# Kernel tuning notes

Hardware: AMD Instinct MI355X
Metric: run time of the kernel (lower is better)

Reference implementation:

```python
import jax, jax.numpy as jnp
import numpy as np

B, S, D, H = 4, 2048, 1024, 16
HD = D // H


def setup_inputs() -> dict:
    key = jax.random.key(0)
    k1, k2, k3 = jax.random.split(key, 3)
    x = jax.random.normal(k1, (B, S, D), dtype=jnp.float32)
    w_qkv = jax.random.normal(k2, (D, 3 * D), dtype=jnp.float32) * (1.0 / np.sqrt(D))
    w_out = jax.random.normal(k3, (D, D), dtype=jnp.float32) * (1.0 / np.sqrt(D))
    return {"x": x, "w_qkv": w_qkv, "w_out": w_out}


def reference(x, w_qkv, w_out):
    bsz, seq_len, d = x.shape
    qkv = x @ w_qkv  # [B, S, 3D]
    q, k, v = jnp.split(qkv, 3, axis=-1)
    # [B, H, S, HD]
    q = q.reshape(bsz, seq_len, H, HD).transpose(0, 2, 1, 3)
    k = k.reshape(bsz, seq_len, H, HD).transpose(0, 2, 1, 3)
    v = v.reshape(bsz, seq_len, H, HD).transpose(0, 2, 1, 3)
    scale = 1.0 / np.sqrt(HD)
    scores = jnp.einsum('bhqd,bhkd->bhqk', q, k) * scale  # [B, H, S, S]
    causal = jnp.tril(jnp.ones((seq_len, seq_len), dtype=bool))
    scores = jnp.where(causal[None, None], scores, -jnp.inf)
    weights = jax.nn.softmax(scores, axis=-1)
    ctx = jnp.einsum('bhqk,bhkd->bhqd', weights, v)
    ctx = ctx.transpose(0, 2, 1, 3).reshape(bsz, seq_len, d)
    return ctx @ w_out
```

## Files before the change

### kernel.cpp

```cpp
#include <hip/hip_runtime.h>
#include <stdint.h>

typedef unsigned short u16;
typedef __attribute__((ext_vector_type(4))) float f32x4;
typedef __attribute__((ext_vector_type(16))) float f32x16;
typedef __attribute__((ext_vector_type(8))) __bf16 bf16x8;
typedef __attribute__((ext_vector_type(8))) u16 u16x8;
typedef __attribute__((ext_vector_type(4))) u16 u16x4;

static constexpr int kB = 4, kS = 2048, kD = 1024, kH = 16, kHD = 64;
static constexpr int M1 = kB * kS;
static constexpr int N1 = 3 * kD;
static constexpr int K1 = kD;

#define SCLF 0.18033688011112042f
#define MFMA32(a, b, c) __builtin_amdgcn_mfma_f32_32x32x16_bf16((a), (b), (c), 0, 0, 0)

union U4 { unsigned u[4]; bf16x8 v; };

__device__ __forceinline__ u16 f2bf(float f) {
  union { float f; uint32_t u; } c; c.f = f;
  uint32_t u = c.u + 0x7FFFu + ((c.u >> 16) & 1u);
  return (u16)(u >> 16);
}

__device__ __forceinline__ unsigned pkbf(float a, float b) {
  union { __bf16 h[2]; unsigned u; } c;
  c.h[0] = (__bf16)a; c.h[1] = (__bf16)b;
  return c.u;
}

__device__ __forceinline__ f32x16 zero16() {
  f32x16 v;
#pragma unroll
  for (int i = 0; i < 16; ++i) v[i] = 0.f;
  return v;
}

__device__ __forceinline__ void gload_lds16(const u16* g, u16* l) {
  __builtin_amdgcn_global_load_lds(
      (const __attribute__((address_space(1))) unsigned int*)g,
      (__attribute__((address_space(3))) unsigned int*)l, 16, 0, 0);
}

__device__ __forceinline__ void packP(const float* pp, int hi, U4& f0, U4& f1) {
  const unsigned qa0 = pkbf(pp[0], pp[1]),   qa1 = pkbf(pp[2], pp[3]);
  const unsigned qb0 = pkbf(pp[4], pp[5]),   qb1 = pkbf(pp[6], pp[7]);
  const unsigned qc0 = pkbf(pp[8], pp[9]),   qc1 = pkbf(pp[10], pp[11]);
  const unsigned qd0 = pkbf(pp[12], pp[13]), qd1 = pkbf(pp[14], pp[15]);
  const unsigned xa0 = __shfl_xor(qa0, 32, 64), xa1 = __shfl_xor(qa1, 32, 64);
  const unsigned xb0 = __shfl_xor(qb0, 32, 64), xb1 = __shfl_xor(qb1, 32, 64);
  const unsigned xc0 = __shfl_xor(qc0, 32, 64), xc1 = __shfl_xor(qc1, 32, 64);
  const unsigned xd0 = __shfl_xor(qd0, 32, 64), xd1 = __shfl_xor(qd1, 32, 64);
  f0.u[0] = hi ? xb0 : qa0; f0.u[1] = hi ? xb1 : qa1;
  f0.u[2] = hi ? qb0 : xa0; f0.u[3] = hi ? qb1 : xa1;
  f1.u[0] = hi ? xd0 : qc0; f1.u[1] = hi ? xd1 : qc1;
  f1.u[2] = hi ? qd0 : xc0; f1.u[3] = hi ? qd1 : xc1;
}

__global__ __launch_bounds__(256) void k_cast_x(const float* __restrict__ x,
                                                u16* __restrict__ o) {
  int i = (blockIdx.x * 256 + threadIdx.x) * 4;
  f32x4 v = *(const f32x4*)(x + i);
  u16x4 r;
  r[0] = f2bf(v[0]); r[1] = f2bf(v[1]); r[2] = f2bf(v[2]); r[3] = f2bf(v[3]);
  *(u16x4*)(o + i) = r;
}

__global__ __launch_bounds__(256) void k_transpose_cast(const float* __restrict__ w,
                                                        u16* __restrict__ wt,
                                                        int K, int N) {
  __shared__ float t[32][33];
  const int n0 = blockIdx.x * 32, k0 = blockIdx.y * 32;
  const int tx = threadIdx.x & 31, ty = threadIdx.x >> 5;
  for (int r = ty; r < 32; r += 8)
    t[r][tx] = w[(size_t)(k0 + r) * N + n0 + tx];
  __syncthreads();
  for (int r = ty; r < 32; r += 8)
    wt[(size_t)(n0 + r) * K + k0 + tx] = f2bf(t[tx][r]);
}

template <int MODE>
__global__ __launch_bounds__(256) void k_gemm_bt(const u16* __restrict__ A,
                                                 const u16* __restrict__ BT,
                                                 u16* __restrict__ obf,
                                                 float* __restrict__ of,
                                                 int M, int N, int K) {
  typedef __attribute__((ext_vector_type(4))) float f4;
  __shared__ __align__(16) u16 As[128 * 32];
  __shared__ __align__(16) u16 Bs[128 * 32];
  const int tid = threadIdx.x;
  const int wave = tid >> 6, lane = tid & 63;
  const int l15 = lane & 15, l16 = lane >> 4;
  const int row0 = blockIdx.y * 128, col0 = blockIdx.x * 128;
  const int wm = (wave >> 1) * 64, wn = (wave & 1) * 64;

  f4 acc[4][4];
#pragma unroll
  for (int i = 0; i < 4; ++i)
#pragma unroll
    for (int j = 0; j < 4; ++j) acc[i][j] = f4{0.f, 0.f, 0.f, 0.f};

  const int e0 = wave * 512 + lane * 8;
  const int r0 = e0 >> 5, c0 = e0 & 31;
  const int e1 = e0 + 2048;
  const int r1 = e1 >> 5, c1 = e1 & 31;
  const u16* Ab = A + (size_t)row0 * K;
  const u16* Bb = BT + (size_t)col0 * K;

  for (int kt = 0; kt < K; kt += 32) {
    gload_lds16(Ab + (size_t)r0 * K + kt + c0, &As[wave * 512]);
    gload_lds16(Ab + (size_t)r1 * K + kt + c1, &As[2048 + wave * 512]);
    gload_lds16(Bb + (size_t)r0 * K + kt + c0, &Bs[wave * 512]);
    gload_lds16(Bb + (size_t)r1 * K + kt + c1, &Bs[2048 + wave * 512]);
    __syncthreads();
    bf16x8 af[4], bfv[4];
#pragma unroll
    for (int f = 0; f < 4; ++f) {
      af[f]  = *(const bf16x8*)&As[(wm + f * 16 + l15) * 32 + l16 * 8];
      bfv[f] = *(const bf16x8*)&Bs[(wn + f * 16 + l15) * 32 + l16 * 8];
    }
#pragma unroll
    for (int fm = 0; fm < 4; ++fm)
#pragma unroll
      for (int fn = 0; fn < 4; ++fn)
        acc[fm][fn] = __builtin_amdgcn_mfma_f32_16x16x32_bf16(af[fm], bfv[fn],
                                                              acc[fm][fn], 0, 0, 0);
    __syncthreads();
  }

#pragma unroll
  for (int fm = 0; fm < 4; ++fm)
#pragma unroll
    for (int fn = 0; fn < 4; ++fn) {
      const int n = col0 + wn + fn * 16 + l15;
#pragma unroll
      for (int j = 0; j < 4; ++j) {
        const int m = row0 + wm + fm * 16 + l16 * 4 + j;
        float v = acc[fm][fn][j];
        if constexpr (MODE == 0) {
          const int which = n >> 10, d = n & 1023;
          const int h = d >> 6, hd = d & 63;
          const int b = m >> 11, s = m & 2047;
          if (which == 0) v *= SCLF;
          obf[((((size_t)which * 4 + b) * 16 + h) * 2048 + s) * 64 + hd] = f2bf(v);
        } else {
          of[(size_t)m * N + n] = v;
        }
      }
    }
}

__global__ __launch_bounds__(256, 2) void k_attn(const u16* __restrict__ Qg,
                                                 const u16* __restrict__ Kg,
                                                 const u16* __restrict__ Vg,
                                                 u16* __restrict__ ctx) {
  __shared__ __align__(16) u16 Ks[2][128 * 64];
  __shared__ __align__(16) unsigned Vt[2][64 * 64];

  const int p = blockIdx.x, bh = blockIdx.y;
  const int bb = bh >> 4, hh = bh & 15;
  const int tid = threadIdx.x;
  const int wave = tid >> 6, lane = tid & 63;
  const int l31 = lane & 31, hi = lane >> 5;

  const u16* Qb = Qg + (size_t)bh * kS * kHD;
  const u16* Kb = Kg + (size_t)bh * kS * kHD;
  const u16* Vb = Vg + (size_t)bh * kS * kHD;

  const int do8 = tid & 7, kpw = tid >> 3;
  const int kkey8 = lane >> 3, ksl = lane & 7;
  const int swzA = (((l31 & 7) ^ (l31 >> 3)) << 2);

  for (int phase = 0; phase < 2; ++phase) {
    const int qsup = phase ? (15 - p) : p;
    const int s0 = qsup * 128;
    const int qstart = s0 + wave * 32;
    const int ntiles = qsup + 1;

    bf16x8 bq[4];
#pragma unroll
    for (int ds = 0; ds < 4; ++ds)
      bq[ds] = *(const bf16x8*)(Qb + (size_t)(qstart + l31) * 64 + ds * 16 + hi * 8);

    f32x16 acco0 = zero16(), acco1 = zero16();
    float mrow = -3e38f, lrowh = 0.f;

    __syncthreads();

    u16x8 va[2], vb[2];
#pragma unroll
    for (int r = 0; r < 2; ++r) {
      const u16* vs = Vb + (size_t)(2 * (kpw + 32 * r)) * 64 + do8 * 8;
      va[r] = *(const u16x8*)vs; vb[r] = *(const u16x8*)(vs + 64);
    }
#pragma unroll
    for (int r = 0; r < 2; ++r)
#pragma unroll
      for (int i = 0; i < 8; ++i) {
        const int d = do8 * 8 + i;
        Vt[0][d * 64 + ((kpw + 32 * r) ^ ((((d & 7) ^ (d >> 3))) << 2))] =
            (unsigned)va[r][i] | ((unsigned)vb[r][i] << 16);
      }
#pragma unroll
    for (int r = 0; r < 2; ++r) {
      const u16* vs = Vb + (size_t)(128 + 2 * (kpw + 32 * r)) * 64 + do8 * 8;
      va[r] = *(const u16x8*)vs; vb[r] = *(const u16x8*)(vs + 64);
    }
#pragma unroll
    for (int r = 0; r < 4; ++r) {
      const int key = wave * 32 + r * 8 + kkey8;
      gload_lds16(Kb + (size_t)key * 64 + (ksl ^ (key & 7)) * 8,
                  &Ks[0][(wave * 4 + r) * 512]);
    }

    for (int t = 0; t < ntiles; ++t) {
      const int kv0 = t * 128;
      __syncthreads();

      if (t + 1 < ntiles) {
        const int nb = (t + 1) & 1;
#pragma unroll
        for (int r = 0; r < 2; ++r)
#pragma unroll
          for (int i = 0; i < 8; ++i) {
            const int d = do8 * 8 + i;
            Vt[nb][d * 64 + ((kpw + 32 * r) ^ ((((d & 7) ^ (d >> 3))) << 2))] =
                (unsigned)va[r][i] | ((unsigned)vb[r][i] << 16);
          }
#pragma unroll
        for (int r = 0; r < 4; ++r) {
          const int key = wave * 32 + r * 8 + kkey8;
          gload_lds16(Kb + (size_t)(kv0 + 128 + key) * 64 + (ksl ^ (key & 7)) * 8,
                      &Ks[nb][(wave * 4 + r) * 512]);
        }
        if (t + 2 < ntiles) {
#pragma unroll
          for (int r = 0; r < 2; ++r) {
            const u16* vs = Vb + (size_t)(kv0 + 256 + 2 * (kpw + 32 * r)) * 64 + do8 * 8;
            va[r] = *(const u16x8*)vs; vb[r] = *(const u16x8*)(vs + 64);
          }
        }
      }

      const u16* Ksb = &Ks[t & 1][0];
      const unsigned* Vtb = &Vt[t & 1][0];
      const int qv = qstart + l31;

#pragma unroll
      for (int h = 0; h < 2; ++h) {
        const int kb = kv0 + 64 * h;
        if (kb > qstart + 31) continue;
        const int krow = 64 * h;
        const bool pres1 = (kb + 32 <= qstart + 31);

        f32x16 st0 = zero16(), st1 = zero16();
        __builtin_amdgcn_s_setprio(1);
#pragma unroll
        for (int ds = 0; ds < 4; ++ds) {
          const int sl = (((ds << 1) | hi) ^ (l31 & 7)) * 8;
          bf16x8 ak0 = *(const bf16x8*)&Ksb[(krow + l31) * 64 + sl];
          st0 = MFMA32(ak0, bq[ds], st0);
          if (pres1) {
            bf16x8 ak1 = *(const bf16x8*)&Ksb[(krow + 32 + l31) * 64 + sl];
            st1 = MFMA32(ak1, bq[ds], st1);
          }
        }
        __builtin_amdgcn_s_setprio(0);

        float tl = -3e38f;
        if (kb + 31 > qstart) {
          const int kb0 = kb + 4 * hi;
#pragma unroll
          for (int r = 0; r < 16; ++r) {
            const int key = kb0 + (r & 3) + 8 * (r >> 2);
            float v = st0[r];
            v = (key <= qv) ? v : -3e38f;
            st0[r] = v;
            tl = fmaxf(tl, v);
          }
        } else {
#pragma unroll
          for (int r = 0; r < 16; ++r) tl = fmaxf(tl, st0[r]);
        }
        if (pres1) {
          if (kb + 63 > qstart) {
            const int kb1 = kb + 32 + 4 * hi;
#pragma unroll
            for (int r = 0; r < 16; ++r) {
              const int key = kb1 + (r & 3) + 8 * (r >> 2);
              float v = st1[r];
              v = (key <= qv) ? v : -3e38f;
              st1[r] = v;
              tl = fmaxf(tl, v);
            }
          } else {
#pragma unroll
            for (int r = 0; r < 16; ++r) tl = fmaxf(tl, st1[r]);
          }
        }

        float mn;
        if (__all(tl <= mrow + 8.0f)) {
          mn = mrow;
        } else {
          const float tj = fmaxf(tl, __shfl_xor(tl, 32, 64));
          mn = fmaxf(mrow, tj);
          const float al = exp2f(mrow - mn);
          mrow = mn;
          lrowh *= al;
#pragma unroll
          for (int r = 0; r < 16; ++r) { acco0[r] *= al; acco1[r] *= al; }
        }

        {
          float pp[16];
#pragma unroll
          for (int r = 0; r < 16; ++r) pp[r] = exp2f(st0[r] - mn);
          const float t0 = (pp[0] + pp[1]) + (pp[2] + pp[3]);
          const float t1 = (pp[4] + pp[5]) + (pp[6] + pp[7]);
          const float t2 = (pp[8] + pp[9]) + (pp[10] + pp[11]);
          const float t3 = (pp[12] + pp[13]) + (pp[14] + pp[15]);
          lrowh += (t0 + t1) + (t2 + t3);
          U4 f0, f1;
          packP(pp, hi, f0, f1);
          const int c0 = 32 * h;
          __builtin_amdgcn_s_setprio(1);
          {
            const int dbase = l31 * 64, sz = swzA;
            const bf16x8 vfa = *(const bf16x8*)&Vtb[dbase + ((c0 + hi * 4) ^ sz)];
            acco0 = MFMA32(vfa, f0.v, acco0);
            const bf16x8 vfb = *(const bf16x8*)&Vtb[dbase + ((c0 + 8 + hi * 4) ^ sz)];
            acco0 = MFMA32(vfb, f1.v, acco0);
          }
          {
            const int dbase = (32 + l31) * 64, sz = swzA ^ 16;
            const bf16x8 vfa = *(const bf16x8*)&Vtb[dbase + ((c0 + hi * 4) ^ sz)];
            acco1 = MFMA32(vfa, f0.v, acco1);
            const bf16x8 vfb = *(const bf16x8*)&Vtb[dbase + ((c0 + 8 + hi * 4) ^ sz)];
            acco1 = MFMA32(vfb, f1.v, acco1);
          }
          __builtin_amdgcn_s_setprio(0);
        }
        if (pres1) {
          float pp[16];
#pragma unroll
          for (int r = 0; r < 16; ++r) pp[r] = exp2f(st1[r] - mn);
          const float t0 = (pp[0] + pp[1]) + (pp[2] + pp[3]);
          const float t1 = (pp[4] + pp[5]) + (pp[6] + pp[7]);
          const float t2 = (pp[8] + pp[9]) + (pp[10] + pp[11]);
          const float t3 = (pp[12] + pp[13]) + (pp[14] + pp[15]);
          lrowh += (t0 + t1) + (t2 + t3);
          U4 f0, f1;
          packP(pp, hi, f0, f1);
          const int c1 = 32 * h + 16;
          __builtin_amdgcn_s_setprio(1);
          {
            const int dbase = l31 * 64, sz = swzA;
            const bf16x8 vfa = *(const bf16x8*)&Vtb[dbase + ((c1 + hi * 4) ^ sz)];
            acco0 = MFMA32(vfa, f0.v, acco0);
            const bf16x8 vfb = *(const bf16x8*)&Vtb[dbase + ((c1 + 8 + hi * 4) ^ sz)];
            acco0 = MFMA32(vfb, f1.v, acco0);
          }
          {
            const int dbase = (32 + l31) * 64, sz = swzA ^ 16;
            const bf16x8 vfa = *(const bf16x8*)&Vtb[dbase + ((c1 + hi * 4) ^ sz)];
            acco1 = MFMA32(vfa, f0.v, acco1);
            const bf16x8 vfb = *(const bf16x8*)&Vtb[dbase + ((c1 + 8 + hi * 4) ^ sz)];
            acco1 = MFMA32(vfb, f1.v, acco1);
          }
          __builtin_amdgcn_s_setprio(0);
        }
      }
    }

    const float lrow = lrowh + __shfl_xor(lrowh, 32, 64);
    const float rl = 1.0f / lrow;
    u16* orow = ctx + ((size_t)bb * kS + (qstart + l31)) * kD + hh * 64;
#pragma unroll
    for (int rq = 0; rq < 4; ++rq) {
      u16x4 pk0, pk1;
#pragma unroll
      for (int c = 0; c < 4; ++c) {
        pk0[c] = f2bf(acco0[rq * 4 + c] * rl);
        pk1[c] = f2bf(acco1[rq * 4 + c] * rl);
      }
      *(u16x4*)&orow[rq * 8 + hi * 4] = pk0;
      *(u16x4*)&orow[32 + rq * 8 + hi * 4] = pk1;
    }
  }
}

extern "C" void kernel_launch(void* const* d_in, const int* in_sizes, int n_in,
                              void* d_out, int out_size, void* d_ws, size_t ws_size,
                              hipStream_t stream) {
  const float* x     = (const float*)d_in[0];
  const float* w_qkv = (const float*)d_in[1];
  const float* w_out = (const float*)d_in[2];
  float* out = (float*)d_out;

  u16* ws    = (u16*)d_ws;
  u16* x_bf  = ws;
  u16* wqkvT = x_bf + (size_t)M1 * K1;
  u16* woutT = wqkvT + (size_t)N1 * K1;
  u16* qkv   = woutT + (size_t)kD * kD;
  u16* ctx   = qkv + (size_t)3 * kB * kH * kS * kHD;

  k_cast_x<<<M1 * K1 / 1024, 256, 0, stream>>>(x, x_bf);
  k_transpose_cast<<<dim3(N1 / 32, K1 / 32), 256, 0, stream>>>(w_qkv, wqkvT, K1, N1);
  k_transpose_cast<<<dim3(kD / 32, kD / 32), 256, 0, stream>>>(w_out, woutT, kD, kD);

  k_gemm_bt<0><<<dim3(N1 / 128, M1 / 128), 256, 0, stream>>>(x_bf, wqkvT, qkv, nullptr,
                                                             M1, N1, K1);

  const u16* Qg = qkv;
  const u16* Kg = qkv + (size_t)kB * kH * kS * kHD;
  const u16* Vg = qkv + (size_t)2 * kB * kH * kS * kHD;
  k_attn<<<dim3(8, kB * kH), 256, 0, stream>>>(Qg, Kg, Vg, ctx);

  k_gemm_bt<1><<<dim3(kD / 128, M1 / 128), 256, 0, stream>>>(ctx, woutT, nullptr, out,
                                                             M1, kD, K1);
}
```

Measured before the change: 212.0 us.

## Split attention into one block per query tile with XCD-aware ordering and smaller KV tiles

```diff
diff --git a/kernel.cpp b/kernel.cpp
--- a/kernel.cpp
+++ b/kernel.cpp
@@ -92,7 +92,11 @@
   const int tid = threadIdx.x;
   const int wave = tid >> 6, lane = tid & 63;
   const int l15 = lane & 15, l16 = lane >> 4;
-  const int row0 = blockIdx.y * 128, col0 = blockIdx.x * 128;
+
+  const int bid = blockIdx.y * gridDim.x + blockIdx.x;
+  const int qch = (gridDim.x * gridDim.y) >> 3;
+  const int swz = (bid & 7) * qch + (bid >> 3);
+  const int row0 = (swz / gridDim.x) * 128, col0 = (swz % gridDim.x) * 128;
   const int wm = (wave >> 1) * 64, wn = (wave & 1) * 64;
 
   f4 acc[4][4];
@@ -151,243 +155,225 @@
     }
 }
 
-__global__ __launch_bounds__(256, 2) void k_attn(const u16* __restrict__ Qg,
+__global__ __launch_bounds__(256, 4) void k_attn(const u16* __restrict__ Qg,
                                                  const u16* __restrict__ Kg,
                                                  const u16* __restrict__ Vg,
                                                  u16* __restrict__ ctx) {
-  __shared__ __align__(16) u16 Ks[2][128 * 64];
-  __shared__ __align__(16) unsigned Vt[2][64 * 64];
-
-  const int p = blockIdx.x, bh = blockIdx.y;
+  __shared__ __align__(16) u16 Ks[2][64 * 64];
+  __shared__ __align__(16) unsigned Vt[2][64 * 32];
+
+  const int bid = blockIdx.x;
+  const int xcd = bid & 7, idx = bid >> 3;
+  const int bh = xcd * 8 + (idx >> 4);
+  const int qsup = 15 - (idx & 15);
   const int bb = bh >> 4, hh = bh & 15;
   const int tid = threadIdx.x;
   const int wave = tid >> 6, lane = tid & 63;
   const int l31 = lane & 31, hi = lane >> 5;
+  const int s0 = qsup * 128;
+  const int qstart = s0 + wave * 32;
+  const int ntiles = 2 * qsup + 2;
 
   const u16* Qb = Qg + (size_t)bh * kS * kHD;
   const u16* Kb = Kg + (size_t)bh * kS * kHD;
   const u16* Vb = Vg + (size_t)bh * kS * kHD;
 
-  const int do8 = tid & 7, kpw = tid >> 3;
+  const int do8 = tid & 7, kp = tid >> 3;
   const int kkey8 = lane >> 3, ksl = lane & 7;
   const int swzA = (((l31 & 7) ^ (l31 >> 3)) << 2);
 
-  for (int phase = 0; phase < 2; ++phase) {
-    const int qsup = phase ? (15 - p) : p;
-    const int s0 = qsup * 128;
-    const int qstart = s0 + wave * 32;
-    const int ntiles = qsup + 1;
-
-    bf16x8 bq[4];
-#pragma unroll
-    for (int ds = 0; ds < 4; ++ds)
-      bq[ds] = *(const bf16x8*)(Qb + (size_t)(qstart + l31) * 64 + ds * 16 + hi * 8);
-
-    f32x16 acco0 = zero16(), acco1 = zero16();
-    float mrow = -3e38f, lrowh = 0.f;
-
+  unsigned voff[8];
+#pragma unroll
+  for (int i = 0; i < 8; ++i) {
+    const int d = do8 * 8 + i;
+    voff[i] = d * 32 + (kp ^ ((((d & 7) ^ (d >> 3))) << 2));
+  }
+
+  bf16x8 bq[4];
+#pragma unroll
+  for (int ds = 0; ds < 4; ++ds)
+    bq[ds] = *(const bf16x8*)(Qb + (size_t)(qstart + l31) * 64 + ds * 16 + hi * 8);
+
+  f32x16 acco0 = zero16(), acco1 = zero16();
+  float mrow = -3e38f, lrowh = 0.f;
+
+  u16x8 va, vb;
+  {
+    const u16* vs = Vb + (size_t)(2 * kp) * 64 + do8 * 8;
+    va = *(const u16x8*)vs; vb = *(const u16x8*)(vs + 64);
+  }
+#pragma unroll
+  for (int i = 0; i < 8; ++i)
+    Vt[0][voff[i]] = (unsigned)va[i] | ((unsigned)vb[i] << 16);
+  {
+    const u16* vs = Vb + (size_t)(64 + 2 * kp) * 64 + do8 * 8;
+    va = *(const u16x8*)vs; vb = *(const u16x8*)(vs + 64);
+  }
+#pragma unroll
+  for (int rep = 0; rep < 2; ++rep) {
+    const int key = wave * 16 + rep * 8 + kkey8;
+    gload_lds16(Kb + (size_t)key * 64 + (ksl ^ (key & 7)) * 8,
+                &Ks[0][(wave * 2 + rep) * 512]);
+  }
+
+  for (int t = 0; t < ntiles; ++t) {
+    const int kv0 = t * 64;
     __syncthreads();
 
-    u16x8 va[2], vb[2];
-#pragma unroll
-    for (int r = 0; r < 2; ++r) {
-      const u16* vs = Vb + (size_t)(2 * (kpw + 32 * r)) * 64 + do8 * 8;
-      va[r] = *(const u16x8*)vs; vb[r] = *(const u16x8*)(vs + 64);
-    }
-#pragma unroll
-    for (int r = 0; r < 2; ++r)
-#pragma unroll
-      for (int i = 0; i < 8; ++i) {
-        const int d = do8 * 8 + i;
-        Vt[0][d * 64 + ((kpw + 32 * r) ^ ((((d & 7) ^ (d >> 3))) << 2))] =
-            (unsigned)va[r][i] | ((unsigned)vb[r][i] << 16);
-      }
-#pragma unroll
-    for (int r = 0; r < 2; ++r) {
-      const u16* vs = Vb + (size_t)(128 + 2 * (kpw + 32 * r)) * 64 + do8 * 8;
-      va[r] = *(const u16x8*)vs; vb[r] = *(const u16x8*)(vs + 64);
-    }
-#pragma unroll
-    for (int r = 0; r < 4; ++r) {
-      const int key = wave * 32 + r * 8 + kkey8;
-      gload_lds16(Kb + (size_t)key * 64 + (ksl ^ (key & 7)) * 8,
-                  &Ks[0][(wave * 4 + r) * 512]);
-    }
-
-    for (int t = 0; t < ntiles; ++t) {
-      const int kv0 = t * 128;
-      __syncthreads();
-
-      if (t + 1 < ntiles) {
-        const int nb = (t + 1) & 1;
-#pragma unroll
-        for (int r = 0; r < 2; ++r)
-#pragma unroll
-          for (int i = 0; i < 8; ++i) {
-            const int d = do8 * 8 + i;
-            Vt[nb][d * 64 + ((kpw + 32 * r) ^ ((((d & 7) ^ (d >> 3))) << 2))] =
-                (unsigned)va[r][i] | ((unsigned)vb[r][i] << 16);
-          }
-#pragma unroll
-        for (int r = 0; r < 4; ++r) {
-          const int key = wave * 32 + r * 8 + kkey8;
-          gload_lds16(Kb + (size_t)(kv0 + 128 + key) * 64 + (ksl ^ (key & 7)) * 8,
-                      &Ks[nb][(wave * 4 + r) * 512]);
+    if (t + 1 < ntiles) {
+      const int nb = (t + 1) & 1;
+#pragma unroll
+      for (int i = 0; i < 8; ++i)
+        Vt[nb][voff[i]] = (unsigned)va[i] | ((unsigned)vb[i] << 16);
+#pragma unroll
+      for (int rep = 0; rep < 2; ++rep) {
+        const int key = wave * 16 + rep * 8 + kkey8;
+        gload_lds16(Kb + (size_t)(kv0 + 64 + key) * 64 + (ksl ^ (key & 7)) * 8,
+                    &Ks[nb][(wave * 2 + rep) * 512]);
+      }
+      if (t + 2 < ntiles) {
+        const u16* vs = Vb + (size_t)(kv0 + 128 + 2 * kp) * 64 + do8 * 8;
+        va = *(const u16x8*)vs; vb = *(const u16x8*)(vs + 64);
+      }
+    }
+
+    if (kv0 > qstart + 31) continue;
+
+    const u16* Ksb = &Ks[t & 1][0];
+    const unsigned* Vtb = &Vt[t & 1][0];
+    const int qv = qstart + l31;
+    const bool pres1 = (kv0 + 32 <= qstart + 31);
+
+    f32x16 st0 = zero16(), st1 = zero16();
+    __builtin_amdgcn_s_setprio(1);
+#pragma unroll
+    for (int ds = 0; ds < 4; ++ds) {
+      const int sl = (((ds << 1) | hi) ^ (l31 & 7)) * 8;
+      bf16x8 ak0 = *(const bf16x8*)&Ksb[l31 * 64 + sl];
+      st0 = MFMA32(ak0, bq[ds], st0);
+      if (pres1) {
+        bf16x8 ak1 = *(const bf16x8*)&Ksb[(32 + l31) * 64 + sl];
+        st1 = MFMA32(ak1, bq[ds], st1);
+      }
+    }
+    __builtin_amdgcn_s_setprio(0);
+
+    float tl = -3e38f;
+    if (kv0 + 31 > qstart) {
+      const int kb0 = kv0 + 4 * hi;
+#pragma unroll
+      for (int r = 0; r < 16; ++r) {
+        const int key = kb0 + (r & 3) + 8 * (r >> 2);
+        float v = st0[r];
+        v = (key <= qv) ? v : -3e38f;
+        st0[r] = v;
+        tl = fmaxf(tl, v);
+      }
+    } else {
+#pragma unroll
+      for (int r = 0; r < 16; ++r) tl = fmaxf(tl, st0[r]);
+    }
+    if (pres1) {
+      if (kv0 + 63 > qstart) {
+        const int kb1 = kv0 + 32 + 4 * hi;
+#pragma unroll
+        for (int r = 0; r < 16; ++r) {
+          const int key = kb1 + (r & 3) + 8 * (r >> 2);
+          float v = st1[r];
+          v = (key <= qv) ? v : -3e38f;
+          st1[r] = v;
+          tl = fmaxf(tl, v);
         }
-        if (t + 2 < ntiles) {
-#pragma unroll
-          for (int r = 0; r < 2; ++r) {
-            const u16* vs = Vb + (size_t)(kv0 + 256 + 2 * (kpw + 32 * r)) * 64 + do8 * 8;
-            va[r] = *(const u16x8*)vs; vb[r] = *(const u16x8*)(vs + 64);
-          }
-        }
-      }
-
-      const u16* Ksb = &Ks[t & 1][0];
-      const unsigned* Vtb = &Vt[t & 1][0];
-      const int qv = qstart + l31;
-
-#pragma unroll
-      for (int h = 0; h < 2; ++h) {
-        const int kb = kv0 + 64 * h;
-        if (kb > qstart + 31) continue;
-        const int krow = 64 * h;
-        const bool pres1 = (kb + 32 <= qstart + 31);
-
-        f32x16 st0 = zero16(), st1 = zero16();
-        __builtin_amdgcn_s_setprio(1);
-#pragma unroll
-        for (int ds = 0; ds < 4; ++ds) {
-          const int sl = (((ds << 1) | hi) ^ (l31 & 7)) * 8;
-          bf16x8 ak0 = *(const bf16x8*)&Ksb[(krow + l31) * 64 + sl];
-          st0 = MFMA32(ak0, bq[ds], st0);
-          if (pres1) {
-            bf16x8 ak1 = *(const bf16x8*)&Ksb[(krow + 32 + l31) * 64 + sl];
-            st1 = MFMA32(ak1, bq[ds], st1);
-          }
-        }
-        __builtin_amdgcn_s_setprio(0);
-
-        float tl = -3e38f;
-        if (kb + 31 > qstart) {
-          const int kb0 = kb + 4 * hi;
-#pragma unroll
-          for (int r = 0; r < 16; ++r) {
-            const int key = kb0 + (r & 3) + 8 * (r >> 2);
-            float v = st0[r];
-            v = (key <= qv) ? v : -3e38f;
-            st0[r] = v;
-            tl = fmaxf(tl, v);
-          }
-        } else {
-#pragma unroll
-          for (int r = 0; r < 16; ++r) tl = fmaxf(tl, st0[r]);
-        }
-        if (pres1) {
-          if (kb + 63 > qstart) {
-            const int kb1 = kb + 32 + 4 * hi;
-#pragma unroll
-            for (int r = 0; r < 16; ++r) {
-              const int key = kb1 + (r & 3) + 8 * (r >> 2);
-              float v = st1[r];
-              v = (key <= qv) ? v : -3e38f;
-              st1[r] = v;
-              tl = fmaxf(tl, v);
-            }
-          } else {
-#pragma unroll
-            for (int r = 0; r < 16; ++r) tl = fmaxf(tl, st1[r]);
-          }
-        }
-
-        float mn;
-        if (__all(tl <= mrow + 8.0f)) {
-          mn = mrow;
-        } else {
-          const float tj = fmaxf(tl, __shfl_xor(tl, 32, 64));
-          mn = fmaxf(mrow, tj);
-          const float al = exp2f(mrow - mn);
-          mrow = mn;
-          lrowh *= al;
-#pragma unroll
-          for (int r = 0; r < 16; ++r) { acco0[r] *= al; acco1[r] *= al; }
-        }
-
-        {
-          float pp[16];
-#pragma unroll
-          for (int r = 0; r < 16; ++r) pp[r] = exp2f(st0[r] - mn);
-          const float t0 = (pp[0] + pp[1]) + (pp[2] + pp[3]);
-          const float t1 = (pp[4] + pp[5]) + (pp[6] + pp[7]);
-          const float t2 = (pp[8] + pp[9]) + (pp[10] + pp[11]);
-          const float t3 = (pp[12] + pp[13]) + (pp[14] + pp[15]);
-          lrowh += (t0 + t1) + (t2 + t3);
-          U4 f0, f1;
-          packP(pp, hi, f0, f1);
-          const int c0 = 32 * h;
-          __builtin_amdgcn_s_setprio(1);
-          {
-            const int dbase = l31 * 64, sz = swzA;
-            const bf16x8 vfa = *(const bf16x8*)&Vtb[dbase + ((c0 + hi * 4) ^ sz)];
-            acco0 = MFMA32(vfa, f0.v, acco0);
-            const bf16x8 vfb = *(const bf16x8*)&Vtb[dbase + ((c0 + 8 + hi * 4) ^ sz)];
-            acco0 = MFMA32(vfb, f1.v, acco0);
-          }
-          {
-            const int dbase = (32 + l31) * 64, sz = swzA ^ 16;
-            const bf16x8 vfa = *(const bf16x8*)&Vtb[dbase + ((c0 + hi * 4) ^ sz)];
-            acco1 = MFMA32(vfa, f0.v, acco1);
-            const bf16x8 vfb = *(const bf16x8*)&Vtb[dbase + ((c0 + 8 + hi * 4) ^ sz)];
-            acco1 = MFMA32(vfb, f1.v, acco1);
-          }
-          __builtin_amdgcn_s_setprio(0);
-        }
-        if (pres1) {
-          float pp[16];
-#pragma unroll
-          for (int r = 0; r < 16; ++r) pp[r] = exp2f(st1[r] - mn);
-          const float t0 = (pp[0] + pp[1]) + (pp[2] + pp[3]);
-          const float t1 = (pp[4] + pp[5]) + (pp[6] + pp[7]);
-          const float t2 = (pp[8] + pp[9]) + (pp[10] + pp[11]);
-          const float t3 = (pp[12] + pp[13]) + (pp[14] + pp[15]);
-          lrowh += (t0 + t1) + (t2 + t3);
-          U4 f0, f1;
-          packP(pp, hi, f0, f1);
-          const int c1 = 32 * h + 16;
-          __builtin_amdgcn_s_setprio(1);
-          {
-            const int dbase = l31 * 64, sz = swzA;
-            const bf16x8 vfa = *(const bf16x8*)&Vtb[dbase + ((c1 + hi * 4) ^ sz)];
-            acco0 = MFMA32(vfa, f0.v, acco0);
-            const bf16x8 vfb = *(const bf16x8*)&Vtb[dbase + ((c1 + 8 + hi * 4) ^ sz)];
-            acco0 = MFMA32(vfb, f1.v, acco0);
-          }
-          {
-            const int dbase = (32 + l31) * 64, sz = swzA ^ 16;
-            const bf16x8 vfa = *(const bf16x8*)&Vtb[dbase + ((c1 + hi * 4) ^ sz)];
-            acco1 = MFMA32(vfa, f0.v, acco1);
-            const bf16x8 vfb = *(const bf16x8*)&Vtb[dbase + ((c1 + 8 + hi * 4) ^ sz)];
-            acco1 = MFMA32(vfb, f1.v, acco1);
-          }
-          __builtin_amdgcn_s_setprio(0);
-        }
-      }
-    }
-
-    const float lrow = lrowh + __shfl_xor(lrowh, 32, 64);
-    const float rl = 1.0f / lrow;
-    u16* orow = ctx + ((size_t)bb * kS + (qstart + l31)) * kD + hh * 64;
-#pragma unroll
-    for (int rq = 0; rq < 4; ++rq) {
-      u16x4 pk0, pk1;
-#pragma unroll
-      for (int c = 0; c < 4; ++c) {
-        pk0[c] = f2bf(acco0[rq * 4 + c] * rl);
-        pk1[c] = f2bf(acco1[rq * 4 + c] * rl);
-      }
-      *(u16x4*)&orow[rq * 8 + hi * 4] = pk0;
-      *(u16x4*)&orow[32 + rq * 8 + hi * 4] = pk1;
-    }
+      } else {
+#pragma unroll
+        for (int r = 0; r < 16; ++r) tl = fmaxf(tl, st1[r]);
+      }
+    }
+
+    float mn;
+    if (__all(tl <= mrow + 8.0f)) {
+      mn = mrow;
+    } else {
+      const float tj = fmaxf(tl, __shfl_xor(tl, 32, 64));
+      mn = fmaxf(mrow, tj);
+      const float al = exp2f(mrow - mn);
+      mrow = mn;
+      lrowh *= al;
+#pragma unroll
+      for (int r = 0; r < 16; ++r) { acco0[r] *= al; acco1[r] *= al; }
+    }
+
+    {
+      float pp[16];
+#pragma unroll
+      for (int r = 0; r < 16; ++r) pp[r] = exp2f(st0[r] - mn);
+      const float t0 = (pp[0] + pp[1]) + (pp[2] + pp[3]);
+      const float t1 = (pp[4] + pp[5]) + (pp[6] + pp[7]);
+      const float t2 = (pp[8] + pp[9]) + (pp[10] + pp[11]);
+      const float t3 = (pp[12] + pp[13]) + (pp[14] + pp[15]);
+      lrowh += (t0 + t1) + (t2 + t3);
+      U4 f0, f1;
+      packP(pp, hi, f0, f1);
+      __builtin_amdgcn_s_setprio(1);
+      {
+        const int dbase = l31 * 32, sz = swzA;
+        const bf16x8 vfa = *(const bf16x8*)&Vtb[dbase + ((hi * 4) ^ sz)];
+        acco0 = MFMA32(vfa, f0.v, acco0);
+        const bf16x8 vfb = *(const bf16x8*)&Vtb[dbase + ((8 + hi * 4) ^ sz)];
+        acco0 = MFMA32(vfb, f1.v, acco0);
+      }
+      {
+        const int dbase = (32 + l31) * 32, sz = swzA ^ 16;
+        const bf16x8 vfa = *(const bf16x8*)&Vtb[dbase + ((hi * 4) ^ sz)];
+        acco1 = MFMA32(vfa, f0.v, acco1);
+        const bf16x8 vfb = *(const bf16x8*)&Vtb[dbase + ((8 + hi * 4) ^ sz)];
+        acco1 = MFMA32(vfb, f1.v, acco1);
+      }
+      __builtin_amdgcn_s_setprio(0);
+    }
+    if (pres1) {
+      float pp[16];
+#pragma unroll
+      for (int r = 0; r < 16; ++r) pp[r] = exp2f(st1[r] - mn);
+      const float t0 = (pp[0] + pp[1]) + (pp[2] + pp[3]);
+      const float t1 = (pp[4] + pp[5]) + (pp[6] + pp[7]);
+      const float t2 = (pp[8] + pp[9]) + (pp[10] + pp[11]);
+      const float t3 = (pp[12] + pp[13]) + (pp[14] + pp[15]);
+      lrowh += (t0 + t1) + (t2 + t3);
+      U4 f0, f1;
+      packP(pp, hi, f0, f1);
+      __builtin_amdgcn_s_setprio(1);
+      {
+        const int dbase = l31 * 32, sz = swzA;
+        const bf16x8 vfa = *(const bf16x8*)&Vtb[dbase + ((16 + hi * 4) ^ sz)];
+        acco0 = MFMA32(vfa, f0.v, acco0);
+        const bf16x8 vfb = *(const bf16x8*)&Vtb[dbase + ((24 + hi * 4) ^ sz)];
+        acco0 = MFMA32(vfb, f1.v, acco0);
+      }
+      {
+        const int dbase = (32 + l31) * 32, sz = swzA ^ 16;
+        const bf16x8 vfa = *(const bf16x8*)&Vtb[dbase + ((16 + hi * 4) ^ sz)];
+        acco1 = MFMA32(vfa, f0.v, acco1);
+        const bf16x8 vfb = *(const bf16x8*)&Vtb[dbase + ((24 + hi * 4) ^ sz)];
+        acco1 = MFMA32(vfb, f1.v, acco1);
+      }
+      __builtin_amdgcn_s_setprio(0);
+    }
+  }
+
+  const float lrow = lrowh + __shfl_xor(lrowh, 32, 64);
+  const float rl = 1.0f / lrow;
+  u16* orow = ctx + ((size_t)bb * kS + (qstart + l31)) * kD + hh * 64;
+#pragma unroll
+  for (int rq = 0; rq < 4; ++rq) {
+    u16x4 pk0, pk1;
+#pragma unroll
+    for (int c = 0; c < 4; ++c) {
+      pk0[c] = f2bf(acco0[rq * 4 + c] * rl);
+      pk1[c] = f2bf(acco1[rq * 4 + c] * rl);
+    }
+    *(u16x4*)&orow[rq * 8 + hi * 4] = pk0;
+    *(u16x4*)&orow[32 + rq * 8 + hi * 4] = pk1;
   }
 }
 
@@ -416,7 +402,7 @@
   const u16* Qg = qkv;
   const u16* Kg = qkv + (size_t)kB * kH * kS * kHD;
   const u16* Vg = qkv + (size_t)2 * kB * kH * kS * kHD;
-  k_attn<<<dim3(8, kB * kH), 256, 0, stream>>>(Qg, Kg, Vg, ctx);
+  k_attn<<<dim3(1024), 256, 0, stream>>>(Qg, Kg, Vg, ctx);
 
   k_gemm_bt<1><<<dim3(kD / 128, M1 / 128), 256, 0, stream>>>(ctx, woutT, nullptr, out,
                                                              M1, kD, K1);
```

Result: slower. 351.0 us (+65.6%).
